# Kernel optimization log

Hardware: AMD Instinct MI355X
Metric: run time of the kernel (lower is better)

## Reference

```python
import jax, jax.numpy as jnp
import numpy as np

# Sizes
N, T, P, D = 1000, 4, 10, 13          # nodes, point types, edge types (T*(T+1)/2), basis dim per point
F, H, EA, K, E = 128, 128, 16, 64, 20000  # node feat, edge hidden, edge attr/feat, edge op bottleneck, edges
I_NODE = D * (D + 1) // 2             # 91: symmetric ('ij=ji') self-block irreps dim
I_EDGE = D * D                        # 169: generic ('ij') block irreps dim
AVG_NEIGH = 20.0


def setup_inputs() -> dict:
    ks = jax.random.split(jax.random.key(0), 16)
    Fin = H + 2 * F                   # edge-op input: [edge_msg, node_h_i, node_h_j]
    return {
        'node_feats': jax.random.normal(ks[0], (N, F), jnp.float32),
        'node_attrs': jax.random.uniform(ks[1], (N, T), dtype=jnp.float32),
        'edge_feats': jax.random.normal(ks[2], (E, EA), jnp.float32),
        'edge_attrs': jax.random.normal(ks[3], (E, EA), jnp.float32),
        'edge_index': jax.random.randint(ks[4], (2, E), 0, N),
        'node_types': jax.random.randint(ks[5], (N,), 0, T),
        'edge_types': jax.random.randint(ks[6], (E,), 0, P),
        'W_msg': jax.random.normal(ks[7], (F, F), jnp.float32) / np.float32(np.sqrt(F)),
        'W_attr': jax.random.normal(ks[8], (T, F), jnp.float32) / np.float32(np.sqrt(T)),
        'W_em': jax.random.normal(ks[9], (2 * F + 2 * EA, H), jnp.float32) / np.float32(np.sqrt(2 * F + 2 * EA)),
        'W_proj': jax.random.normal(ks[10], (Fin, K), jnp.float32) / np.float32(np.sqrt(Fin)),
        'W_node': jax.random.normal(ks[11], (T, F, I_NODE), jnp.float32) / np.float32(np.sqrt(F)),
        'W_edge': jax.random.normal(ks[12], (P, K, I_EDGE), jnp.float32) / np.float32(np.sqrt(K)),
        'cob_node': jax.random.normal(ks[13], (T, I_NODE, D, D), jnp.float32) / np.float32(D),
        'cob_edge': jax.random.normal(ks[14], (P, I_EDGE, D, D), jnp.float32) / np.float32(D),
    }


def reference(node_feats, node_attrs, edge_feats, edge_attrs, edge_index, node_types,
              edge_types, W_msg, W_attr, W_em, W_proj, W_node, W_edge, cob_node, cob_edge):
    src, dst = edge_index[0], edge_index[1]
    # --- node message passing (NodeMessageBlock, simplified linear-aggregate form) ---
    m = node_feats @ W_msg                                             # [N, F]
    agg = jax.ops.segment_sum(m[src], dst, num_segments=N) \
        + jax.ops.segment_sum(m[dst], src, num_segments=N)             # symmetric edge list: both dirs
    node_h = node_feats + agg / AVG_NEIGH + node_attrs @ W_attr        # [N, F]
    # --- edge messages (EdgeMessageBlock, simplified) ---
    e_in = jnp.concatenate([node_h[src], node_h[dst], edge_feats, edge_attrs], axis=-1)
    edge_msg = jnp.tanh(e_in @ W_em)                                   # [E, H]
    # --- self-interaction blocks: per-type gather -> op -> einsum('ni,ixy->nxy', ., cob) ---
    node_irred = jnp.einsum('nf,nfi->ni', node_h, W_node[node_types])  # [N, I_NODE]
    node_blocks = jnp.einsum('ni,nixy->nxy', node_irred, cob_node[node_types])  # [N, D, D]
    # --- interaction blocks: per-edge-type op + change of basis, transpose-symmetrized ---
    onehot = jax.nn.one_hot(edge_types, P, dtype=node_feats.dtype)     # [E, P] type selector

    def edge_block(a, b):
        h = jnp.concatenate([edge_msg, a, b], axis=-1) @ W_proj        # [E, K]
        irr = jnp.einsum('epi,ep->ei', jnp.einsum('ek,pki->epi', h, W_edge), onehot)  # [E, I_EDGE]
        return jnp.einsum('epxy,ep->exy', jnp.einsum('ei,pixy->epxy', irr, cob_edge), onehot)  # [E, D, D]

    blk_ij = edge_block(node_h[src], node_h[dst])
    blk_ji = edge_block(node_h[dst], node_h[src])
    edge_blocks = 0.5 * (blk_ij + jnp.swapaxes(blk_ji, -1, -2))        # symm_transpose
    # --- scatter blocks into the dense symmetric block matrix ---
    off = jnp.arange(D)
    nidx = jnp.arange(N)[:, None] * D + off                            # [N, D] diagonal block rows/cols
    rs = src[:, None] * D + off                                        # [E, D]
    cs = dst[:, None] * D + off
    M = jnp.zeros((N * D, N * D), node_feats.dtype)
    M = M.at[nidx[:, :, None], nidx[:, None, :]].add(node_blocks)
    M = M.at[rs[:, :, None], cs[:, None, :]].add(edge_blocks)
    M = M.at[cs[:, :, None], rs[:, None, :]].add(jnp.swapaxes(edge_blocks, -1, -2))
    return M
```

## Files before the change

kernel.cpp:

```cpp
#include <hip/hip_runtime.h>
#include <cmath>

#define NN   1000
#define TT   4
#define PP   10
#define DD   13
#define FF   128
#define HH   128
#define EAA  16
#define KDIM 64
#define EE   20000
#define I_NODE 91
#define I_EDGE 169
#define MROW  13000
#define ROW4  3250

#define WS_EBLK  0L
#define WS_M     0L
#define WS_AGG   128000L
#define WS_NBLK  3380000L
#define WS_V1    3549000L
#define WS_V2    3677000L
#define WS_U     3805000L
#define WS_WCOMB 3933000L
#define WS_WNC   4041160L
#define WS_INT   4127688L
#define IO_CNT   0
#define IO_OFF   1000
#define IO_CUR   2001
#define IO_ADJ   3001

#define NB_CE   640
#define NB_CN   512
#define NB_MSG  1000
#define NB_FRONT (NB_CE + NB_CN + NB_MSG + 1)

__global__ __launch_bounds__(256) void k_front(
    const float* __restrict__ We, const float* __restrict__ cobE,
    const float* __restrict__ Wn, const float* __restrict__ cobN,
    const float* __restrict__ nf, const float* __restrict__ Wmsg,
    float* __restrict__ Wcomb, float* __restrict__ Wnc,
    float* __restrict__ m, float* __restrict__ agg, int* __restrict__ cnt) {
  int b = blockIdx.x, t = threadIdx.x;
  if (b < NB_CE) {
    if (t < I_EDGE) {
      int pk = b, p = pk >> 6;
      float acc = 0.f;
      const float* wrow = We + pk * I_EDGE;
      const float* crow = cobE + p * I_EDGE * I_EDGE + t;
      for (int i = 0; i < I_EDGE; ++i) acc += wrow[i] * crow[i * I_EDGE];
      Wcomb[pk * I_EDGE + t] = acc;
    }
  } else if (b < NB_CE + NB_CN) {
    if (t < I_EDGE) {
      int tf = b - NB_CE, ty = tf >> 7;
      float acc = 0.f;
      const float* wrow = Wn + tf * I_NODE;
      const float* crow = cobN + ty * I_NODE * I_EDGE + t;
      for (int i = 0; i < I_NODE; ++i) acc += wrow[i] * crow[i * I_EDGE];
      Wnc[tf * I_EDGE + t] = acc;
    }
  } else if (b < NB_CE + NB_CN + NB_MSG) {
    int n = b - (NB_CE + NB_CN);
    __shared__ float row[FF];
    if (t < FF) row[t] = nf[n * FF + t];
    __syncthreads();
    if (t < FF) {
      float acc = 0.f;
#pragma unroll 8
      for (int f = 0; f < FF; ++f) acc += row[f] * Wmsg[f * FF + t];
      m[n * FF + t] = acc;
    } else {
      agg[n * FF + (t - FF)] = 0.f;
    }
  } else {
    for (int i = t; i < NN; i += 256) cnt[i] = 0;
  }
}

__global__ __launch_bounds__(256) void k_scatter(
    const float* __restrict__ m, const int* __restrict__ src,
    const int* __restrict__ dst, float* __restrict__ agg,
    int* __restrict__ cnt) {
  int idx = blockIdx.x * 256 + threadIdx.x;
  if (idx >= EE * FF) return;
  int e = idx >> 7, j = idx & 127;
  int s = src[e], d = dst[e];
  if (j == 0) { atomicAdd(&cnt[s], 1); atomicAdd(&cnt[d], 1); }
  atomicAdd(&agg[d * FF + j], m[s * FF + j]);
  atomicAdd(&agg[s * FF + j], m[d * FF + j]);
}

__global__ __launch_bounds__(192) void k_nodes(
    const float* __restrict__ nf, const float* __restrict__ agg,
    const float* __restrict__ na, const float* __restrict__ Wattr,
    const float* __restrict__ Wem, const float* __restrict__ Wproj,
    const int* __restrict__ ntype, const float* __restrict__ Wnc,
    float* __restrict__ V1, float* __restrict__ V2, float* __restrict__ U,
    float* __restrict__ nblk, const int* __restrict__ cnt,
    int* __restrict__ off, int* __restrict__ cur) {
  int t = threadIdx.x;
  if (blockIdx.x == NN) {
    __shared__ int sc[192];
    int base = t * 6, run = 0, loc[6];
#pragma unroll
    for (int i = 0; i < 6; ++i) {
      int v = (base + i < NN) ? cnt[base + i] : 0;
      loc[i] = run; run += v;
    }
    sc[t] = run;
    __syncthreads();
    for (int dd = 1; dd < 192; dd <<= 1) {
      int v = (t >= dd) ? sc[t - dd] : 0;
      __syncthreads();
      sc[t] += v;
      __syncthreads();
    }
    int excl = (t == 0) ? 0 : sc[t - 1];
#pragma unroll
    for (int i = 0; i < 6; ++i)
      if (base + i < NN) { int o = excl + loc[i]; off[base + i] = o; cur[base + i] = o; }
    if (t == 0) off[NN] = sc[191];
    return;
  }
  int n = blockIdx.x;
  int ty = ntype[n];
  __shared__ float row[FF];
  if (t < FF) {
    float a = 0.f;
#pragma unroll
    for (int q = 0; q < TT; ++q) a += na[n * TT + q] * Wattr[q * FF + t];
    row[t] = nf[n * FF + t] + agg[n * FF + t] * (1.0f / 20.0f) + a;
  }
  __syncthreads();
  if (t < FF) {
    float v1 = 0.f, v2 = 0.f;
#pragma unroll 4
    for (int f = 0; f < FF; ++f) {
      float x = row[f];
      v1 += x * Wem[f * HH + t];
      v2 += x * Wem[(FF + f) * HH + t];
    }
    V1[n * HH + t] = v1;
    V2[n * HH + t] = v2;
    int k = t & 63, half = t >> 6;
    const float* W = Wproj + (FF + half * FF) * KDIM + k;
    float u = 0.f;
#pragma unroll 4
    for (int f = 0; f < FF; ++f) u += row[f] * W[f * KDIM];
    U[n * 128 + t] = u;
  }
  if (t < I_EDGE) {
    float acc = 0.f;
    const float* W = Wnc + ty * FF * I_EDGE + t;
#pragma unroll 4
    for (int f = 0; f < FF; ++f) acc += row[f] * W[f * I_EDGE];
    nblk[n * I_EDGE + t] = acc;
  }
}

#define EB 4
__global__ __launch_bounds__(768) void k_edge_all(
    const float* __restrict__ V1, const float* __restrict__ V2,
    const float* __restrict__ U, const float* __restrict__ ef,
    const float* __restrict__ ea, const int* __restrict__ src,
    const int* __restrict__ dst, const int* __restrict__ etype,
    const float* __restrict__ Wem, const float* __restrict__ Wproj,
    const float* __restrict__ Wcomb, float* __restrict__ eblk,
    int* __restrict__ cur, int* __restrict__ adj) {
  int t = threadIdx.x;
  int ei = threadIdx.y;
  int e = blockIdx.x * EB + ei;
  int s = src[e], d = dst[e], p = etype[e];
  __shared__ __align__(16) float efa[EB][32];
  __shared__ __align__(16) float em[EB][HH];
  __shared__ __align__(16) float hp[EB][2][KDIM];
  __shared__ __align__(16) float h[EB][2][KDIM];
  __shared__ __align__(16) float tji[EB][I_EDGE];

  if (t == 0) {
    int pos = atomicAdd(&cur[s], 1); adj[pos] = 2 * e;
    int pos2 = atomicAdd(&cur[d], 1); adj[pos2] = 2 * e + 1;
  }
  if (t < 32) efa[ei][t] = (t < 16) ? ef[e * EAA + t] : ea[e * EAA + (t - 16)];
  __syncthreads();

  if (t < HH) {
    float acc = V1[s * HH + t] + V2[d * HH + t];
#pragma unroll
    for (int c = 0; c < 32; ++c) acc += efa[ei][c] * Wem[(256 + c) * HH + t];
    em[ei][t] = tanhf(acc);
  }
  __syncthreads();

  if (t < 128) {
    int k = t & 63, half = t >> 6;
    float hm = 0.f;
    for (int f = half * 64; f < half * 64 + 64; f += 4) {
      float4 mv = *(const float4*)&em[ei][f];
      hm += mv.x * Wproj[(f + 0) * KDIM + k] + mv.y * Wproj[(f + 1) * KDIM + k]
          + mv.z * Wproj[(f + 2) * KDIM + k] + mv.w * Wproj[(f + 3) * KDIM + k];
    }
    hp[ei][half][k] = hm;
  }
  __syncthreads();
  if (t < KDIM) {
    float hm = hp[ei][0][t] + hp[ei][1][t];
    h[ei][0][t] = hm + U[s * 128 + t] + U[d * 128 + 64 + t];
    h[ei][1][t] = hm + U[d * 128 + t] + U[s * 128 + 64 + t];
  }
  __syncthreads();

  float bij = 0.f, bji = 0.f;
  if (t < I_EDGE) {
    const float* W = Wcomb + p * KDIM * I_EDGE + t;
    for (int k = 0; k < KDIM; k += 4) {
      float4 hi = *(const float4*)&h[ei][0][k];
      float4 hj = *(const float4*)&h[ei][1][k];
      float w0 = W[(k + 0) * I_EDGE], w1 = W[(k + 1) * I_EDGE];
      float w2 = W[(k + 2) * I_EDGE], w3 = W[(k + 3) * I_EDGE];
      bij += hi.x * w0 + hi.y * w1 + hi.z * w2 + hi.w * w3;
      bji += hj.x * w0 + hj.y * w1 + hj.z * w2 + hj.w * w3;
    }
    tji[ei][t] = bji;
  }
  __syncthreads();
  if (t < I_EDGE) {
    int x = t / DD, y = t % DD;
    eblk[(size_t)e * I_EDGE + t] = 0.5f * (bij + tji[ei][y * DD + x]);
  }
}

#define MAXS 72
__global__ __launch_bounds__(256) void k_assemble(
    const float* __restrict__ eblk, const float* __restrict__ nblk,
    const int* __restrict__ off, const int* __restrict__ adj,
    const int* __restrict__ src, const int* __restrict__ dst,
    float* __restrict__ M) {
  int n = blockIdx.x, t = threadIdx.x;
  __shared__ float blk[MAXS][I_EDGE];
  __shared__ signed char map8[13008];
  __shared__ int s_ed[MAXS];
  __shared__ short s_other[MAXS];
  int* map32 = (int*)map8;
  for (int i = t; i < 3252; i += 256) map32[i] = -1;
  int o0 = off[n], o1 = off[n + 1];
  int nent = 1 + (o1 - o0);
  int ns = nent < MAXS ? nent : MAXS;
  for (int i = t; i < ns; i += 256) {
    int ed, other;
    if (i == 0) { ed = -1; other = n; }
    else { ed = adj[o0 + i - 1]; int e = ed >> 1; other = (ed & 1) ? src[e] : dst[e]; }
    s_ed[i] = ed; s_other[i] = (short)other;
  }
  __syncthreads();
  for (int j = t; j < ns * DD; j += 256) {
    int i = j / DD, c = j - i * DD;
    map8[(int)s_other[i] * DD + c] = (signed char)i;
  }
  for (int j = t; j < ns * I_EDGE; j += 256) {
    int i = j / I_EDGE, cell = j - i * I_EDGE;
    int ed = s_ed[i];
    float v;
    if (ed < 0)      v = nblk[n * I_EDGE + cell];
    else if (ed & 1) v = eblk[(size_t)(ed >> 1) * I_EDGE + (cell % DD) * DD + cell / DD];
    else             v = eblk[(size_t)(ed >> 1) * I_EDGE + cell];
    blk[i][cell] = v;
  }
  __syncthreads();
  for (int j = t; j < ns * I_EDGE; j += 256) {
    int i = j / I_EDGE, cell = j - i * I_EDGE;
    int cloc = cell % DD;
    int w = map8[(int)s_other[i] * DD + cloc];
    if (w != i) atomicAdd(&blk[w][cell], blk[i][cell]);
  }
  __syncthreads();
  float4* M4 = (float4*)M;
  for (int r = 0; r < DD; ++r) {
    float4* rowp = M4 + (size_t)(n * DD + r) * ROW4;
    int rb = r * DD;
    for (int c4 = t; c4 < ROW4; c4 += 256) {
      int mp = map32[c4];
      float4 v = make_float4(0.f, 0.f, 0.f, 0.f);
      if (mp != -1) {
        int col = c4 * 4;
        signed char m0 = (signed char)(mp & 0xff);
        signed char m1 = (signed char)((mp >> 8) & 0xff);
        signed char m2 = (signed char)((mp >> 16) & 0xff);
        signed char m3 = (signed char)((mp >> 24) & 0xff);
        if (m0 >= 0) v.x = blk[m0][rb + (col + 0) % DD];
        if (m1 >= 0) v.y = blk[m1][rb + (col + 1) % DD];
        if (m2 >= 0) v.z = blk[m2][rb + (col + 2) % DD];
        if (m3 >= 0) v.w = blk[m3][rb + (col + 3) % DD];
      }
      rowp[c4] = v;
    }
  }
  if (nent > MAXS) {
    __threadfence_block();
    __syncthreads();
    if (t < I_EDGE) {
      int x = t / DD, y = t - (t / DD) * DD;
      for (int i = MAXS; i < nent; ++i) {
        int ed = adj[o0 + i - 1]; int e = ed >> 1;
        int other = (ed & 1) ? src[e] : dst[e];
        float v = (ed & 1) ? eblk[(size_t)e * I_EDGE + y * DD + x]
                           : eblk[(size_t)e * I_EDGE + x * DD + y];
        M[(size_t)(n * DD + x) * MROW + other * DD + y] += v;
      }
    }
  }
}

extern "C" void kernel_launch(void* const* d_in, const int* in_sizes, int n_in,
                              void* d_out, int out_size, void* d_ws, size_t ws_size,
                              hipStream_t stream) {
  const float* node_feats = (const float*)d_in[0];
  const float* node_attrs = (const float*)d_in[1];
  const float* edge_feats = (const float*)d_in[2];
  const float* edge_attrs = (const float*)d_in[3];
  const int*   edge_index = (const int*)d_in[4];
  const int*   node_types = (const int*)d_in[5];
  const int*   edge_types = (const int*)d_in[6];
  const float* W_msg  = (const float*)d_in[7];
  const float* W_attr = (const float*)d_in[8];
  const float* W_em   = (const float*)d_in[9];
  const float* W_proj = (const float*)d_in[10];
  const float* W_node = (const float*)d_in[11];
  const float* W_edge = (const float*)d_in[12];
  const float* cob_node = (const float*)d_in[13];
  const float* cob_edge = (const float*)d_in[14];

  float* M  = (float*)d_out;
  float* ws = (float*)d_ws;
  float* eblk  = ws + WS_EBLK;
  float* m_buf = ws + WS_M;
  float* agg   = ws + WS_AGG;
  float* nblk  = ws + WS_NBLK;
  float* V1    = ws + WS_V1;
  float* V2    = ws + WS_V2;
  float* U     = ws + WS_U;
  float* Wcomb = ws + WS_WCOMB;
  float* Wnc   = ws + WS_WNC;
  int*   iw    = (int*)(ws + WS_INT);
  int*   cnt   = iw + IO_CNT;
  int*   off   = iw + IO_OFF;
  int*   cur   = iw + IO_CUR;
  int*   adj   = iw + IO_ADJ;

  const int* src = edge_index;
  const int* dst = edge_index + EE;

  k_front   <<<NB_FRONT, 256, 0, stream>>>(W_edge, cob_edge, W_node, cob_node,
                                           node_feats, W_msg, Wcomb, Wnc,
                                           m_buf, agg, cnt);
  k_scatter <<<(EE * FF) / 256, 256, 0, stream>>>(m_buf, src, dst, agg, cnt);
  k_nodes   <<<NN + 1, 192, 0, stream>>>(node_feats, agg, node_attrs, W_attr,
                                         W_em, W_proj, node_types, Wnc,
                                         V1, V2, U, nblk, cnt, off, cur);
  k_edge_all<<<dim3(EE / EB), dim3(192, 4), 0, stream>>>(V1, V2, U, edge_feats,
                                                         edge_attrs, src, dst,
                                                         edge_types, W_em, W_proj,
                                                         Wcomb, eblk, cur, adj);
  k_assemble<<<NN, 256, 0, stream>>>(eblk, nblk, off, adj, src, dst, M);
}
```

Before: 954.0 us.

## Replace atomic feature scatter with CSR gather and split edge kernel

Node aggregation no longer uses per-element float atomics over all edges. The CSR adjacency (count, scan, fill) is now built before the node kernel, and each node gathers its neighbours' messages directly. The edge pipeline is split into a message kernel and a block kernel. The message kernel processes 8 edges per block, keeps Wem columns in registers and reuses each Wproj load across 4 edges. This adds two small launches and an intermediate hmsg buffer in exchange for removing roughly 5M atomics and redundant weight loads.

```diff
diff --git a/kernel.cpp b/kernel.cpp
--- a/kernel.cpp
+++ b/kernel.cpp
@@ -15,16 +15,16 @@
 #define MROW  13000
 #define ROW4  3250
 
-#define WS_EBLK  0L
-#define WS_M     0L
-#define WS_AGG   128000L
-#define WS_NBLK  3380000L
-#define WS_V1    3549000L
-#define WS_V2    3677000L
-#define WS_U     3805000L
-#define WS_WCOMB 3933000L
-#define WS_WNC   4041160L
-#define WS_INT   4127688L
+#define WS_MBUF  0L
+#define WS_HMSG  0L
+#define WS_NBLK  1280000L
+#define WS_V1    1449000L
+#define WS_V2    1577000L
+#define WS_U     1705000L
+#define WS_WCOMB 1833000L
+#define WS_WNC   1941160L
+#define WS_INT   2027688L
+#define WS_EBLK  2070696L
 #define IO_CNT   0
 #define IO_OFF   1000
 #define IO_CUR   2001
@@ -40,7 +40,7 @@
     const float* __restrict__ Wn, const float* __restrict__ cobN,
     const float* __restrict__ nf, const float* __restrict__ Wmsg,
     float* __restrict__ Wcomb, float* __restrict__ Wnc,
-    float* __restrict__ m, float* __restrict__ agg, int* __restrict__ cnt) {
+    float* __restrict__ m, int* __restrict__ cnt) {
   int b = blockIdx.x, t = threadIdx.x;
   if (b < NB_CE) {
     if (t < I_EDGE) {
@@ -70,67 +70,80 @@
 #pragma unroll 8
       for (int f = 0; f < FF; ++f) acc += row[f] * Wmsg[f * FF + t];
       m[n * FF + t] = acc;
-    } else {
-      agg[n * FF + (t - FF)] = 0.f;
     }
   } else {
     for (int i = t; i < NN; i += 256) cnt[i] = 0;
   }
 }
 
-__global__ __launch_bounds__(256) void k_scatter(
-    const float* __restrict__ m, const int* __restrict__ src,
-    const int* __restrict__ dst, float* __restrict__ agg,
+__global__ __launch_bounds__(256) void k_count(
+    const int* __restrict__ src, const int* __restrict__ dst,
     int* __restrict__ cnt) {
-  int idx = blockIdx.x * 256 + threadIdx.x;
-  if (idx >= EE * FF) return;
-  int e = idx >> 7, j = idx & 127;
-  int s = src[e], d = dst[e];
-  if (j == 0) { atomicAdd(&cnt[s], 1); atomicAdd(&cnt[d], 1); }
-  atomicAdd(&agg[d * FF + j], m[s * FF + j]);
-  atomicAdd(&agg[s * FF + j], m[d * FF + j]);
+  int e = blockIdx.x * 256 + threadIdx.x;
+  if (e >= EE) return;
+  atomicAdd(&cnt[src[e]], 1);
+  atomicAdd(&cnt[dst[e]], 1);
+}
+
+__global__ __launch_bounds__(256) void k_scan(
+    const int* __restrict__ cnt, int* __restrict__ off, int* __restrict__ cur) {
+  int t = threadIdx.x;
+  __shared__ int sc[256];
+  int base = t * 4, run = 0, loc[4];
+#pragma unroll
+  for (int i = 0; i < 4; ++i) {
+    int v = (base + i < NN) ? cnt[base + i] : 0;
+    loc[i] = run; run += v;
+  }
+  sc[t] = run;
+  __syncthreads();
+  for (int dd = 1; dd < 256; dd <<= 1) {
+    int v = (t >= dd) ? sc[t - dd] : 0;
+    __syncthreads();
+    sc[t] += v;
+    __syncthreads();
+  }
+  int excl = (t == 0) ? 0 : sc[t - 1];
+#pragma unroll
+  for (int i = 0; i < 4; ++i)
+    if (base + i < NN) { int o = excl + loc[i]; off[base + i] = o; cur[base + i] = o; }
+  if (t == 0) off[NN] = sc[255];
+}
+
+__global__ __launch_bounds__(256) void k_adj(
+    const int* __restrict__ src, const int* __restrict__ dst,
+    int* __restrict__ cur, int* __restrict__ adj) {
+  int e = blockIdx.x * 256 + threadIdx.x;
+  if (e >= EE) return;
+  int p1 = atomicAdd(&cur[src[e]], 1); adj[p1] = 2 * e;
+  int p2 = atomicAdd(&cur[dst[e]], 1); adj[p2] = 2 * e + 1;
 }
 
 __global__ __launch_bounds__(192) void k_nodes(
-    const float* __restrict__ nf, const float* __restrict__ agg,
+    const float* __restrict__ nf, const float* __restrict__ m,
     const float* __restrict__ na, const float* __restrict__ Wattr,
     const float* __restrict__ Wem, const float* __restrict__ Wproj,
     const int* __restrict__ ntype, const float* __restrict__ Wnc,
+    const int* __restrict__ off, const int* __restrict__ adj,
+    const int* __restrict__ src, const int* __restrict__ dst,
     float* __restrict__ V1, float* __restrict__ V2, float* __restrict__ U,
-    float* __restrict__ nblk, const int* __restrict__ cnt,
-    int* __restrict__ off, int* __restrict__ cur) {
-  int t = threadIdx.x;
-  if (blockIdx.x == NN) {
-    __shared__ int sc[192];
-    int base = t * 6, run = 0, loc[6];
-#pragma unroll
-    for (int i = 0; i < 6; ++i) {
-      int v = (base + i < NN) ? cnt[base + i] : 0;
-      loc[i] = run; run += v;
-    }
-    sc[t] = run;
-    __syncthreads();
-    for (int dd = 1; dd < 192; dd <<= 1) {
-      int v = (t >= dd) ? sc[t - dd] : 0;
-      __syncthreads();
-      sc[t] += v;
-      __syncthreads();
-    }
-    int excl = (t == 0) ? 0 : sc[t - 1];
-#pragma unroll
-    for (int i = 0; i < 6; ++i)
-      if (base + i < NN) { int o = excl + loc[i]; off[base + i] = o; cur[base + i] = o; }
-    if (t == 0) off[NN] = sc[191];
-    return;
-  }
-  int n = blockIdx.x;
+    float* __restrict__ nblk) {
+  int n = blockIdx.x, t = threadIdx.x;
   int ty = ntype[n];
   __shared__ float row[FF];
   if (t < FF) {
     float a = 0.f;
 #pragma unroll
     for (int q = 0; q < TT; ++q) a += na[n * TT + q] * Wattr[q * FF + t];
-    row[t] = nf[n * FF + t] + agg[n * FF + t] * (1.0f / 20.0f) + a;
+    float g = 0.f;
+    int o0 = off[n], o1 = off[n + 1];
+    for (int o = o0; o < o1; ++o) {
+      int ed = adj[o];
+      int e = ed >> 1;
+      int other = (ed & 1) ? src[e] : dst[e];
+      g += m[other * FF + t];
+    }
+    row[t] = nf[n * FF + t] + g * (1.0f / 20.0f) + a;
   }
   __syncthreads();
   if (t < FF) {
@@ -159,58 +172,72 @@
   }
 }
 
-#define EB 4
-__global__ __launch_bounds__(768) void k_edge_all(
+#define EPB 8
+__global__ __launch_bounds__(128) void k_edge_msg(
     const float* __restrict__ V1, const float* __restrict__ V2,
-    const float* __restrict__ U, const float* __restrict__ ef,
-    const float* __restrict__ ea, const int* __restrict__ src,
-    const int* __restrict__ dst, const int* __restrict__ etype,
+    const float* __restrict__ ef, const float* __restrict__ ea,
+    const int* __restrict__ src, const int* __restrict__ dst,
     const float* __restrict__ Wem, const float* __restrict__ Wproj,
-    const float* __restrict__ Wcomb, float* __restrict__ eblk,
-    int* __restrict__ cur, int* __restrict__ adj) {
+    float* __restrict__ hmsg) {
+  int e0 = blockIdx.x * EPB;
+  int j = threadIdx.x;
+  __shared__ float efa[EPB][32];
+  __shared__ float em[EPB][HH];
+  for (int i = j; i < EPB * 32; i += 128) {
+    int e = i >> 5, c = i & 31;
+    efa[e][c] = (c < 16) ? ef[(e0 + e) * EAA + c] : ea[(e0 + e) * EAA + (c - 16)];
+  }
+  __syncthreads();
+  float wcol[32];
+#pragma unroll
+  for (int c = 0; c < 32; ++c) wcol[c] = Wem[(256 + c) * HH + j];
+#pragma unroll
+  for (int e = 0; e < EPB; ++e) {
+    int s = src[e0 + e], d = dst[e0 + e];
+    float acc = V1[s * HH + j] + V2[d * HH + j];
+#pragma unroll
+    for (int c = 0; c < 32; ++c) acc += efa[e][c] * wcol[c];
+    em[e][j] = tanhf(acc);
+  }
+  __syncthreads();
+  int k = j & 63, half = j >> 6;
+  float a0 = 0.f, a1 = 0.f, a2 = 0.f, a3 = 0.f;
+  for (int f = 0; f < HH; f += 4) {
+    float4 m0 = *(const float4*)&em[half + 0][f];
+    float4 m1 = *(const float4*)&em[half + 2][f];
+    float4 m2 = *(const float4*)&em[half + 4][f];
+    float4 m3 = *(const float4*)&em[half + 6][f];
+    float w0 = Wproj[(f + 0) * KDIM + k], w1 = Wproj[(f + 1) * KDIM + k];
+    float w2 = Wproj[(f + 2) * KDIM + k], w3 = Wproj[(f + 3) * KDIM + k];
+    a0 += m0.x * w0 + m0.y * w1 + m0.z * w2 + m0.w * w3;
+    a1 += m1.x * w0 + m1.y * w1 + m1.z * w2 + m1.w * w3;
+    a2 += m2.x * w0 + m2.y * w1 + m2.z * w2 + m2.w * w3;
+    a3 += m3.x * w0 + m3.y * w1 + m3.z * w2 + m3.w * w3;
+  }
+  hmsg[(e0 + half + 0) * KDIM + k] = a0;
+  hmsg[(e0 + half + 2) * KDIM + k] = a1;
+  hmsg[(e0 + half + 4) * KDIM + k] = a2;
+  hmsg[(e0 + half + 6) * KDIM + k] = a3;
+}
+
+#define EB2 4
+__global__ __launch_bounds__(768) void k_edge_blk(
+    const float* __restrict__ U, const float* __restrict__ hmsg,
+    const int* __restrict__ src, const int* __restrict__ dst,
+    const int* __restrict__ etype, const float* __restrict__ Wcomb,
+    float* __restrict__ eblk) {
   int t = threadIdx.x;
   int ei = threadIdx.y;
-  int e = blockIdx.x * EB + ei;
+  int e = blockIdx.x * EB2 + ei;
   int s = src[e], d = dst[e], p = etype[e];
-  __shared__ __align__(16) float efa[EB][32];
-  __shared__ __align__(16) float em[EB][HH];
-  __shared__ __align__(16) float hp[EB][2][KDIM];
-  __shared__ __align__(16) float h[EB][2][KDIM];
-  __shared__ __align__(16) float tji[EB][I_EDGE];
-
-  if (t == 0) {
-    int pos = atomicAdd(&cur[s], 1); adj[pos] = 2 * e;
-    int pos2 = atomicAdd(&cur[d], 1); adj[pos2] = 2 * e + 1;
-  }
-  if (t < 32) efa[ei][t] = (t < 16) ? ef[e * EAA + t] : ea[e * EAA + (t - 16)];
-  __syncthreads();
-
-  if (t < HH) {
-    float acc = V1[s * HH + t] + V2[d * HH + t];
-#pragma unroll
-    for (int c = 0; c < 32; ++c) acc += efa[ei][c] * Wem[(256 + c) * HH + t];
-    em[ei][t] = tanhf(acc);
-  }
-  __syncthreads();
-
+  __shared__ __align__(16) float h[EB2][2][KDIM];
+  __shared__ __align__(16) float tji[EB2][I_EDGE];
   if (t < 128) {
-    int k = t & 63, half = t >> 6;
-    float hm = 0.f;
-    for (int f = half * 64; f < half * 64 + 64; f += 4) {
-      float4 mv = *(const float4*)&em[ei][f];
-      hm += mv.x * Wproj[(f + 0) * KDIM + k] + mv.y * Wproj[(f + 1) * KDIM + k]
-          + mv.z * Wproj[(f + 2) * KDIM + k] + mv.w * Wproj[(f + 3) * KDIM + k];
-    }
-    hp[ei][half][k] = hm;
-  }
-  __syncthreads();
-  if (t < KDIM) {
-    float hm = hp[ei][0][t] + hp[ei][1][t];
-    h[ei][0][t] = hm + U[s * 128 + t] + U[d * 128 + 64 + t];
-    h[ei][1][t] = hm + U[d * 128 + t] + U[s * 128 + 64 + t];
-  }
-  __syncthreads();
-
+    int k = t & 63, w = t >> 6;
+    int a = w ? d : s, b = w ? s : d;
+    h[ei][w][k] = hmsg[e * KDIM + k] + U[a * 128 + k] + U[b * 128 + 64 + k];
+  }
+  __syncthreads();
   float bij = 0.f, bji = 0.f;
   if (t < I_EDGE) {
     const float* W = Wcomb + p * KDIM * I_EDGE + t;
@@ -333,9 +360,8 @@
 
   float* M  = (float*)d_out;
   float* ws = (float*)d_ws;
-  float* eblk  = ws + WS_EBLK;
-  float* m_buf = ws + WS_M;
-  float* agg   = ws + WS_AGG;
+  float* m_buf = ws + WS_MBUF;
+  float* hmsg  = ws + WS_HMSG;
   float* nblk  = ws + WS_NBLK;
   float* V1    = ws + WS_V1;
   float* V2    = ws + WS_V2;
@@ -347,20 +373,23 @@
   int*   off   = iw + IO_OFF;
   int*   cur   = iw + IO_CUR;
   int*   adj   = iw + IO_ADJ;
+  float* eblk  = ws + WS_EBLK;
 
   const int* src = edge_index;
   const int* dst = edge_index + EE;
 
   k_front   <<<NB_FRONT, 256, 0, stream>>>(W_edge, cob_edge, W_node, cob_node,
                                            node_feats, W_msg, Wcomb, Wnc,
-                                           m_buf, agg, cnt);
-  k_scatter <<<(EE * FF) / 256, 256, 0, stream>>>(m_buf, src, dst, agg, cnt);
-  k_nodes   <<<NN + 1, 192, 0, stream>>>(node_feats, agg, node_attrs, W_attr,
-                                         W_em, W_proj, node_types, Wnc,
-                                         V1, V2, U, nblk, cnt, off, cur);
-  k_edge_all<<<dim3(EE / EB), dim3(192, 4), 0, stream>>>(V1, V2, U, edge_feats,
-                                                         edge_attrs, src, dst,
-                                                         edge_types, W_em, W_proj,
-                                                         Wcomb, eblk, cur, adj);
+                                           m_buf, cnt);
+  k_count   <<<(EE + 255) / 256, 256, 0, stream>>>(src, dst, cnt);
+  k_scan    <<<1, 256, 0, stream>>>(cnt, off, cur);
+  k_adj     <<<(EE + 255) / 256, 256, 0, stream>>>(src, dst, cur, adj);
+  k_nodes   <<<NN, 192, 0, stream>>>(node_feats, m_buf, node_attrs, W_attr,
+                                     W_em, W_proj, node_types, Wnc,
+                                     off, adj, src, dst, V1, V2, U, nblk);
+  k_edge_msg<<<EE / EPB, 128, 0, stream>>>(V1, V2, edge_feats, edge_attrs, src, dst,
+                                           W_em, W_proj, hmsg);
+  k_edge_blk<<<dim3(EE / EB2), dim3(192, 4), 0, stream>>>(U, hmsg, src, dst,
+                                                          edge_types, Wcomb, eblk);
   k_assemble<<<NN, 256, 0, stream>>>(eblk, nblk, off, adj, src, dst, M);
 }
```

Result: no change. 938.2 us (-1.7%).
